# Performance work log

Hardware: AMD Instinct MI355X
Metric: run time of the kernel (lower is better)

The kernel has to match this reference:

```python
import jax, jax.numpy as jnp
import numpy as np

B, T, D, H, O = 256, 256, 256, 1024, 256


def setup_inputs() -> dict:
    key = jax.random.key(0)
    ks = jax.random.split(key, 4)
    x = jax.random.normal(ks[0], (B, T, D), dtype=jnp.float32)
    # Glorot-ish scaling to keep gates/tanh out of saturation
    Wx = jax.random.normal(ks[1], (D + O, 4 * H), dtype=jnp.float32) * 0.05
    Wh = jax.random.normal(ks[2], (H, 4 * H), dtype=jnp.float32) * 0.05
    b = jnp.zeros((4 * H,), dtype=jnp.float32)
    Wd = jax.random.normal(ks[3], (H, O), dtype=jnp.float32) * 0.05
    bd = jnp.zeros((O,), dtype=jnp.float32)
    return {"x": x, "Wx": Wx, "Wh": Wh, "b": b, "Wd": Wd, "bd": bd}


def reference(x, Wx, Wh, b, Wd, bd):
    """Autoregressive LSTM cell unrolled over time with lax.scan.

    Each step: concat(input_t, prev_dense_output) -> LSTMCell (Keras gate
    order i,f,c,o) -> Dense+tanh -> output fed back next step.
    """
    Bz = x.shape[0]
    Hh = Wh.shape[0]
    Oo = Wd.shape[1]
    h0 = jnp.zeros((Bz, Hh), dtype=x.dtype)
    c0 = jnp.zeros((Bz, Hh), dtype=x.dtype)
    y0 = jnp.zeros((Bz, Oo), dtype=x.dtype)  # initial prev_output

    def step(carry, xt):
        h, c, y = carry
        combined = jnp.concatenate([xt, y], axis=-1)  # [B, D+O]
        z = combined @ Wx + h @ Wh + b                # [B, 4H]
        i, f, g, o = jnp.split(z, 4, axis=-1)
        i = jax.nn.sigmoid(i)
        f = jax.nn.sigmoid(f)
        g = jnp.tanh(g)
        o = jax.nn.sigmoid(o)
        c_new = f * c + i * g
        h_new = o * jnp.tanh(c_new)
        y_new = jnp.tanh(h_new @ Wd + bd)             # Dense(tanh)
        return (h_new, c_new, y_new), y_new

    xs = jnp.swapaxes(x, 0, 1)  # [T, B, D]
    _, ys = jax.lax.scan(step, (h0, c0, y0), xs)
    return jnp.swapaxes(ys, 0, 1)  # [B, T, O]
```

## Files before the change

### kernel.cpp

```cpp
#include <hip/hip_runtime.h>


typedef _Float16 f16x8 __attribute__((ext_vector_type(8)));
typedef _Float16 f16x4 __attribute__((ext_vector_type(4)));
typedef float f32x4 __attribute__((ext_vector_type(4)));

#define TSTEPS 256
#define HID 1024
#define OUTD 256
#define KF 1536
#define KA 1280
#define NBLK 256
#define RSLOTS 16
#define SLOTE (256 * KA)

#define RING_OFF   0ull
#define WFULLT_OFF 0ull
#define WDT_OFF    12582912ull
#define XH_OFF     13107200ull
#define FLAGS_OFF  46661632ull
#define WS_NEEDED  46678016ull

#define LDS_SLAB_BYTES 98304
#define LDS_WDT_BYTES  32768
#define LDS_ZBUF_BYTES 16896
#define LDS_TOTAL (LDS_SLAB_BYTES + LDS_WDT_BYTES + LDS_ZBUF_BYTES)

#define AGENT __HIP_MEMORY_SCOPE_AGENT

__device__ __forceinline__ float sigf(float x) {
    return 1.0f / (1.0f + __expf(-x));
}
__device__ __forceinline__ float tanhfast(float x) {
    return 1.0f - 2.0f / (__expf(2.0f * x) + 1.0f);
}

__device__ __forceinline__ void garrive(int* flags, int bid, int ep) {
    __syncthreads();
    if (threadIdx.x == 0)
        __hip_atomic_store(flags + bid * 16, ep, __ATOMIC_RELAXED, AGENT);
}
__device__ __forceinline__ void gwait(int* flags, int ep) {
    if (threadIdx.x < 64) {
        int lane = threadIdx.x;
        for (;;) {
            int a0 = __hip_atomic_load(flags + (lane)       * 16, __ATOMIC_RELAXED, AGENT);
            int a1 = __hip_atomic_load(flags + (lane + 64)  * 16, __ATOMIC_RELAXED, AGENT);
            int a2 = __hip_atomic_load(flags + (lane + 128) * 16, __ATOMIC_RELAXED, AGENT);
            int a3 = __hip_atomic_load(flags + (lane + 192) * 16, __ATOMIC_RELAXED, AGENT);
            int m = min(min(a0, a1), min(a2, a3));
            if (m >= ep) break;
            __builtin_amdgcn_s_sleep(1);
        }
    }
    __syncthreads();
}

__global__ void prep_w(const float* __restrict__ Wx, const float* __restrict__ Wh,
                       const float* __restrict__ Wd,
                       _Float16* __restrict__ WfullT, _Float16* __restrict__ WdT) {
    int bid = blockIdx.x;
    if (bid < 4096) {
        int n = bid;
        for (int k = threadIdx.x; k < KF; k += 256) {
            float v;
            if (k < 256)       v = Wx[(size_t)k * 4096 + n];
            else if (k < 1280) v = Wh[(size_t)(k - 256) * 4096 + n];
            else               v = Wx[(size_t)(k - 1024) * 4096 + n];
            WfullT[(size_t)n * KF + k] = (_Float16)v;
        }
    } else {
        int o = bid - 4096;
        for (int k = threadIdx.x; k < HID; k += 256) {
            WdT[(size_t)o * HID + k] = (_Float16)Wd[(size_t)k * OUTD + o];
        }
    }
}

__global__ void prep_x(const float* __restrict__ x, _Float16* __restrict__ xh, int* flags) {
    size_t i0 = ((size_t)blockIdx.x * 256 + threadIdx.x) * 8;
    float4 a = *(const float4*)(x + i0);
    float4 c = *(const float4*)(x + i0 + 4);
    f16x8 v;
    v[0] = (_Float16)a.x; v[1] = (_Float16)a.y; v[2] = (_Float16)a.z; v[3] = (_Float16)a.w;
    v[4] = (_Float16)c.x; v[5] = (_Float16)c.y; v[6] = (_Float16)c.z; v[7] = (_Float16)c.w;
    *(f16x8*)(xh + i0) = v;
    if (blockIdx.x == 0)
        for (int i = threadIdx.x; i < 4096; i += 256) flags[i] = 0;
}

template<int NS, typename AL>
__device__ __forceinline__ void gemmPart(AL&& aload, const _Float16* slab, int kbB,
                                         int rl, int kg, f32x4 (&acc)[2][2]) {
    constexpr int PFD = (NS < 8) ? NS : 8;
    f16x8 pa[PFD][2];
#pragma unroll
    for (int i = 0; i < PFD; ++i) { pa[i][0] = aload(i, 0); pa[i][1] = aload(i, 1); }
    const int sw = rl & 7;
    const _Float16* bb0 = slab + (size_t)rl * 1536;
    const _Float16* bb1 = slab + (size_t)(16 + rl) * 1536;
#pragma unroll
    for (int kk = 0; kk < NS; ++kk) {
        int kblk = kbB + kk * 4 + kg;
        int idx = (kblk ^ sw) * 8;
        f16x8 b0 = *(const f16x8*)(bb0 + idx);
        f16x8 b1 = *(const f16x8*)(bb1 + idx);
        f16x8 a0 = pa[kk % PFD][0];
        f16x8 a1 = pa[kk % PFD][1];
        if (kk + PFD < NS) {
            pa[kk % PFD][0] = aload(kk + PFD, 0);
            pa[kk % PFD][1] = aload(kk + PFD, 1);
        }
        acc[0][0] = __builtin_amdgcn_mfma_f32_16x16x32_f16(a0, b0, acc[0][0], 0, 0, 0);
        acc[0][1] = __builtin_amdgcn_mfma_f32_16x16x32_f16(a0, b1, acc[0][1], 0, 0, 0);
        acc[1][0] = __builtin_amdgcn_mfma_f32_16x16x32_f16(a1, b0, acc[1][0], 0, 0, 0);
        acc[1][1] = __builtin_amdgcn_mfma_f32_16x16x32_f16(a1, b1, acc[1][1], 0, 0, 0);
    }
}

__global__ __launch_bounds__(256, 1) void lstm_persist(
        const _Float16* __restrict__ WfullT, const _Float16* __restrict__ WdT,
        const _Float16* __restrict__ xh, const float* __restrict__ b,
        const float* __restrict__ bd,
        _Float16* __restrict__ ring,
        int* flags, float* __restrict__ out) {
    extern __shared__ char dynsm[];
    _Float16* slab = (_Float16*)dynsm;
    _Float16* wdt  = (_Float16*)(dynsm + LDS_SLAB_BYTES);
    float* zbuf = (float*)(dynsm + LDS_SLAB_BYTES + LDS_WDT_BYTES);

    const int tid = threadIdx.x, bid = blockIdx.x;
    const int w = tid >> 6, lane = tid & 63;
    const int rl = lane & 15, kg = lane >> 4;

    const int bat0 = (bid >> 7) << 7;
    const int n0 = (bid & 127) << 3;
    const int r0 = (bid >> 4) << 4;
    const int c0 = (bid & 15) << 4;

    for (int i = tid; i < 32 * 192; i += 256) {
        int vcol = i / 192, kblk = i % 192;
        int n = (vcol & 3) * 1024 + n0 + (vcol >> 2);
        f16x8 v = *(const f16x8*)(WfullT + (size_t)n * KF + kblk * 8);
        *(f16x8*)(slab + ((size_t)vcol * 192 + (kblk ^ (vcol & 7))) * 8) = v;
    }
    for (int i = tid; i < 16 * 128; i += 256) {
        int wcol = i >> 7, kb = i & 127;
        f16x8 v = *(const f16x8*)(WdT + (size_t)(c0 + wcol) * HID + kb * 8);
        *(f16x8*)(wdt + ((size_t)wcol * 128 + (kb ^ (wcol & 7))) * 8) = v;
    }
    const int trow = tid >> 1;
    const int ccB = (tid & 1) * 4;
    float bb[4][4];
#pragma unroll
    for (int g = 0; g < 4; ++g)
#pragma unroll
        for (int c2 = 0; c2 < 4; ++c2)
            bb[g][c2] = b[g * 1024 + n0 + ccB + c2];
    const float bdv = bd[c0 + (tid & 15)];
    float creg[4] = {0.f, 0.f, 0.f, 0.f};

    garrive(flags, bid, 1);
    gwait(flags, 1);

    const size_t arow = (size_t)(bat0 + w * 32 + rl);

    for (int t = 0; t < TSTEPS; ++t) {
        if ((t & 7) == 0)
            __builtin_amdgcn_fence(__ATOMIC_ACQUIRE, "agent");

        const _Float16* slotR = ring + (size_t)((t + RSLOTS - 1) & (RSLOTS - 1)) * SLOTE;
        _Float16* slotW = ring + (size_t)(t & (RSLOTS - 1)) * SLOTE;

        f32x4 acc[2][2];
#pragma unroll
        for (int mt = 0; mt < 2; ++mt)
#pragma unroll
            for (int nt = 0; nt < 2; ++nt) {
                acc[mt][nt][0] = 0.f; acc[mt][nt][1] = 0.f;
                acc[mt][nt][2] = 0.f; acc[mt][nt][3] = 0.f;
            }

        {
            const _Float16* xb = xh + arow * 65536 + (size_t)t * 256 + kg * 8;
            auto loadX = [&](int kk, int mt) -> f16x8 {
                return *(const f16x8*)(xb + (size_t)mt * 16 * 65536 + kk * 32);
            };
            gemmPart<8>(loadX, slab, 0, rl, kg, acc);

            if (t > 0) {
                const _Float16* hb = slotR + arow * KA + kg * 8;
                auto loadH = [&](int kk, int mt) -> f16x8 {
                    return *(const f16x8*)(hb + (size_t)mt * 16 * KA + kk * 32);
                };
                gemmPart<32>(loadH, slab, 32, rl, kg, acc);
            }
        }

        gwait(flags, 2 * t + 1);

        if (t > 0) {
            const _Float16* yb = slotR + arow * KA + 1024 + kg * 8;
            auto loadY = [&](int kk, int mt) -> f16x8 {
                return *(const f16x8*)(yb + (size_t)mt * 16 * KA + kk * 32);
            };
            gemmPart<8>(loadY, slab, 160, rl, kg, acc);
        }

#pragma unroll
        for (int mt = 0; mt < 2; ++mt)
#pragma unroll
            for (int nt = 0; nt < 2; ++nt)
#pragma unroll
                for (int r = 0; r < 4; ++r) {
                    int zrow = w * 32 + mt * 16 + kg * 4 + r;
                    zbuf[zrow * 33 + nt * 16 + rl] = acc[mt][nt][r];
                }
        __syncthreads();
        {
            union { f16x4 v; unsigned long long u; } hu;
#pragma unroll
            for (int c2 = 0; c2 < 4; ++c2) {
                int cc = ccB + c2;
                float zi = zbuf[trow * 33 + cc * 4 + 0];
                float zf = zbuf[trow * 33 + cc * 4 + 1];
                float zg = zbuf[trow * 33 + cc * 4 + 2];
                float zo = zbuf[trow * 33 + cc * 4 + 3];
                float iv = sigf(zi + bb[0][c2]);
                float fv = sigf(zf + bb[1][c2]);
                float gv = tanhfast(zg + bb[2][c2]);
                float ov = sigf(zo + bb[3][c2]);
                float cnew = fv * creg[c2] + iv * gv;
                creg[c2] = cnew;
                hu.v[c2] = (_Float16)(ov * tanhfast(cnew));
            }
            __hip_atomic_store(
                (unsigned long long*)(slotW + (size_t)(bat0 + trow) * KA + n0 + ccB),
                hu.u, __ATOMIC_RELAXED, AGENT);
        }

        garrive(flags, bid, 2 * t + 2);
        gwait(flags, 2 * t + 2);

        {
            const _Float16* hp = slotW + (size_t)(r0 + rl) * KA + (w << 8) + kg * 8;
            f16x8 ha[8], wa[8];
#pragma unroll
            for (int it = 0; it < 8; ++it)
                ha[it] = *(const f16x8*)(hp + it * 32);
#pragma unroll
            for (int it = 0; it < 8; ++it) {
                int kb = (w << 5) + it * 4 + kg;
                wa[it] = *(const f16x8*)(wdt + ((size_t)rl * 128 + (kb ^ (rl & 7))) * 8);
            }
            f32x4 accB; accB[0] = 0.f; accB[1] = 0.f; accB[2] = 0.f; accB[3] = 0.f;
#pragma unroll
            for (int it = 0; it < 8; ++it)
                accB = __builtin_amdgcn_mfma_f32_16x16x32_f16(ha[it], wa[it], accB, 0, 0, 0);
            float* red = zbuf;
#pragma unroll
            for (int r = 0; r < 4; ++r)
                red[w * 256 + (kg * 4 + r) * 16 + rl] = accB[r];
            __syncthreads();
            int rr = tid >> 4, cc = tid & 15;
            float s = red[rr * 16 + cc] + red[256 + rr * 16 + cc] +
                      red[512 + rr * 16 + cc] + red[768 + rr * 16 + cc];
            float y = tanhfast(s + bdv);
            __hip_atomic_store(out + (size_t)(r0 + rr) * 65536 + (size_t)t * 256 + (c0 + cc),
                               y, __ATOMIC_RELAXED, AGENT);
            union { _Float16 h; unsigned short u; } cv; cv.h = (_Float16)y;
            unsigned short* ys = (unsigned short*)(zbuf + 1024);
            ys[tid] = cv.u;
            __syncthreads();
            if (tid < 64) {
                unsigned long long yv = *(const unsigned long long*)(ys + tid * 4);
                int row = r0 + (tid >> 2), colb = c0 + (tid & 3) * 4;
                __hip_atomic_store(
                    (unsigned long long*)(slotW + (size_t)row * KA + 1024 + colb),
                    yv, __ATOMIC_RELAXED, AGENT);
            }
        }

        garrive(flags, bid, 2 * t + 3);
    }
}

extern "C" void kernel_launch(void* const* d_in, const int* in_sizes, int n_in,
                              void* d_out, int out_size, void* d_ws, size_t ws_size,
                              hipStream_t stream) {
    const float* x  = (const float*)d_in[0];
    const float* Wx = (const float*)d_in[1];
    const float* Wh = (const float*)d_in[2];
    const float* b  = (const float*)d_in[3];
    const float* Wd = (const float*)d_in[4];
    const float* bd = (const float*)d_in[5];
    float* out = (float*)d_out;
    char* ws = (char*)d_ws;
    if (ws_size < WS_NEEDED) return;

    _Float16* WfullT = (_Float16*)(ws + WFULLT_OFF);
    _Float16* WdT    = (_Float16*)(ws + WDT_OFF);
    _Float16* xh     = (_Float16*)(ws + XH_OFF);
    _Float16* ring   = (_Float16*)(ws + RING_OFF);
    int*      flags  = (int*)(ws + FLAGS_OFF);

    static int lds_set = 0;
    if (!lds_set) {
        hipFuncSetAttribute((const void*)lstm_persist,
                            hipFuncAttributeMaxDynamicSharedMemorySize, LDS_TOTAL);
        lds_set = 1;
    }

    prep_w<<<4352, 256, 0, stream>>>(Wx, Wh, Wd, WfullT, WdT);
    prep_x<<<8192, 256, 0, stream>>>(x, xh, flags);
    lstm_persist<<<NBLK, 256, LDS_TOTAL, stream>>>(WfullT, WdT, xh, b, bd, ring, flags, out);
}
```

Measured before the change: 4.832 ms.

## Restructure LSTM step schedule with split h/y flags and half-grid barriers

Reorders each timestep so the dense output phase runs right after h is published. The next step's h-GEMM then overlaps with the y exchange. Separate flag arrays for h and y are used, and each block waits only on the 128 blocks of its batch half instead of all 256. Flags are packed densely instead of padded per cache line, with longer sleep intervals in the polling loops. The aim is to cut global barrier latency per step, at the risk of flag-line contention from the dense packing and coarser wake-up from the longer sleep.

Result: faster. 4.259 ms (-11.9%).

```diff
diff --git a/kernel.cpp b/kernel.cpp
--- a/kernel.cpp
+++ b/kernel.cpp
@@ -19,7 +19,7 @@
 #define WDT_OFF    12582912ull
 #define XH_OFF     13107200ull
 #define FLAGS_OFF  46661632ull
-#define WS_NEEDED  46678016ull
+#define WS_NEEDED  46663680ull
 
 #define LDS_SLAB_BYTES 98304
 #define LDS_WDT_BYTES  32768
@@ -38,19 +38,30 @@
 __device__ __forceinline__ void garrive(int* flags, int bid, int ep) {
     __syncthreads();
     if (threadIdx.x == 0)
-        __hip_atomic_store(flags + bid * 16, ep, __ATOMIC_RELAXED, AGENT);
-}
-__device__ __forceinline__ void gwait(int* flags, int ep) {
+        __hip_atomic_store(flags + bid, ep, __ATOMIC_RELAXED, AGENT);
+}
+__device__ __forceinline__ void gwait(int* flags, int gbase, int ep) {
     if (threadIdx.x < 64) {
         int lane = threadIdx.x;
         for (;;) {
-            int a0 = __hip_atomic_load(flags + (lane)       * 16, __ATOMIC_RELAXED, AGENT);
-            int a1 = __hip_atomic_load(flags + (lane + 64)  * 16, __ATOMIC_RELAXED, AGENT);
-            int a2 = __hip_atomic_load(flags + (lane + 128) * 16, __ATOMIC_RELAXED, AGENT);
-            int a3 = __hip_atomic_load(flags + (lane + 192) * 16, __ATOMIC_RELAXED, AGENT);
-            int m = min(min(a0, a1), min(a2, a3));
-            if (m >= ep) break;
-            __builtin_amdgcn_s_sleep(1);
+            int a0 = __hip_atomic_load(flags + gbase + lane,      __ATOMIC_RELAXED, AGENT);
+            int a1 = __hip_atomic_load(flags + gbase + 64 + lane, __ATOMIC_RELAXED, AGENT);
+            if (min(a0, a1) >= ep) break;
+            __builtin_amdgcn_s_sleep(8);
+        }
+    }
+    __syncthreads();
+}
+__device__ __forceinline__ void gwait256(int* flags, int ep) {
+    if (threadIdx.x < 64) {
+        int lane = threadIdx.x;
+        for (;;) {
+            int a0 = __hip_atomic_load(flags + lane,       __ATOMIC_RELAXED, AGENT);
+            int a1 = __hip_atomic_load(flags + lane + 64,  __ATOMIC_RELAXED, AGENT);
+            int a2 = __hip_atomic_load(flags + lane + 128, __ATOMIC_RELAXED, AGENT);
+            int a3 = __hip_atomic_load(flags + lane + 192, __ATOMIC_RELAXED, AGENT);
+            if (min(min(a0, a1), min(a2, a3)) >= ep) break;
+            __builtin_amdgcn_s_sleep(8);
         }
     }
     __syncthreads();
@@ -85,8 +96,10 @@
     v[0] = (_Float16)a.x; v[1] = (_Float16)a.y; v[2] = (_Float16)a.z; v[3] = (_Float16)a.w;
     v[4] = (_Float16)c.x; v[5] = (_Float16)c.y; v[6] = (_Float16)c.z; v[7] = (_Float16)c.w;
     *(f16x8*)(xh + i0) = v;
-    if (blockIdx.x == 0)
-        for (int i = threadIdx.x; i < 4096; i += 256) flags[i] = 0;
+    if (blockIdx.x == 0) {
+        flags[threadIdx.x] = 0;
+        flags[256 + threadIdx.x] = 0;
+    }
 }
 
 template<int NS, typename AL>
@@ -137,6 +150,10 @@
     const int n0 = (bid & 127) << 3;
     const int r0 = (bid >> 4) << 4;
     const int c0 = (bid & 15) << 4;
+    const int gbase = bid & 128;
+
+    int* hflags = flags;
+    int* yflags = flags + 256;
 
     for (int i = tid; i < 32 * 192; i += 256) {
         int vcol = i / 192, kblk = i % 192;
@@ -160,19 +177,105 @@
     const float bdv = bd[c0 + (tid & 15)];
     float creg[4] = {0.f, 0.f, 0.f, 0.f};
 
-    garrive(flags, bid, 1);
-    gwait(flags, 1);
-
     const size_t arow = (size_t)(bat0 + w * 32 + rl);
+
+    auto epilogue = [&](f32x4 (&A)[2][2], _Float16* slotW) {
+#pragma unroll
+        for (int mt = 0; mt < 2; ++mt)
+#pragma unroll
+            for (int nt = 0; nt < 2; ++nt)
+#pragma unroll
+                for (int r = 0; r < 4; ++r) {
+                    int zrow = w * 32 + mt * 16 + kg * 4 + r;
+                    zbuf[zrow * 33 + nt * 16 + rl] = A[mt][nt][r];
+                }
+        __syncthreads();
+        union { f16x4 v; unsigned long long u; } hu;
+#pragma unroll
+        for (int c2 = 0; c2 < 4; ++c2) {
+            int cc = ccB + c2;
+            float zi = zbuf[trow * 33 + cc * 4 + 0];
+            float zf = zbuf[trow * 33 + cc * 4 + 1];
+            float zg = zbuf[trow * 33 + cc * 4 + 2];
+            float zo = zbuf[trow * 33 + cc * 4 + 3];
+            float iv = sigf(zi + bb[0][c2]);
+            float fv = sigf(zf + bb[1][c2]);
+            float gv = tanhfast(zg + bb[2][c2]);
+            float ov = sigf(zo + bb[3][c2]);
+            float cnew = fv * creg[c2] + iv * gv;
+            creg[c2] = cnew;
+            hu.v[c2] = (_Float16)(ov * tanhfast(cnew));
+        }
+        __hip_atomic_store(
+            (unsigned long long*)(slotW + (size_t)(bat0 + trow) * KA + n0 + ccB),
+            hu.u, __ATOMIC_RELAXED, AGENT);
+    };
+
+    auto phaseB = [&](int t, _Float16* slotT) {
+        const _Float16* hp = slotT + (size_t)(r0 + rl) * KA + (w << 8) + kg * 8;
+        f16x8 ha[8], wa[8];
+#pragma unroll
+        for (int it = 0; it < 8; ++it)
+            ha[it] = *(const f16x8*)(hp + it * 32);
+#pragma unroll
+        for (int it = 0; it < 8; ++it) {
+            int kb = (w << 5) + it * 4 + kg;
+            wa[it] = *(const f16x8*)(wdt + ((size_t)rl * 128 + (kb ^ (rl & 7))) * 8);
+        }
+        f32x4 accB; accB[0] = 0.f; accB[1] = 0.f; accB[2] = 0.f; accB[3] = 0.f;
+#pragma unroll
+        for (int it = 0; it < 8; ++it)
+            accB = __builtin_amdgcn_mfma_f32_16x16x32_f16(ha[it], wa[it], accB, 0, 0, 0);
+        float* red = zbuf;
+#pragma unroll
+        for (int r = 0; r < 4; ++r)
+            red[w * 256 + (kg * 4 + r) * 16 + rl] = accB[r];
+        __syncthreads();
+        int rr = tid >> 4, cc = tid & 15;
+        float s = red[rr * 16 + cc] + red[256 + rr * 16 + cc] +
+                  red[512 + rr * 16 + cc] + red[768 + rr * 16 + cc];
+        float y = tanhfast(s + bdv);
+        out[(size_t)(r0 + rr) * 65536 + (size_t)t * 256 + (c0 + cc)] = y;
+        union { _Float16 h; unsigned short u; } cv; cv.h = (_Float16)y;
+        unsigned short* ys = (unsigned short*)(zbuf + 1024);
+        ys[tid] = cv.u;
+        __syncthreads();
+        if (tid < 64) {
+            unsigned long long yv = *(const unsigned long long*)(ys + tid * 4);
+            int row = r0 + (tid >> 2), colb = c0 + (tid & 3) * 4;
+            __hip_atomic_store(
+                (unsigned long long*)(slotT + (size_t)row * KA + 1024 + colb),
+                yv, __ATOMIC_RELAXED, AGENT);
+        }
+    };
+
+    garrive(hflags, bid, 1);
+    gwait256(hflags, 1);
+
+    f32x4 acc[2][2];
+#pragma unroll
+    for (int mt = 0; mt < 2; ++mt)
+#pragma unroll
+        for (int nt = 0; nt < 2; ++nt) {
+            acc[mt][nt][0] = 0.f; acc[mt][nt][1] = 0.f;
+            acc[mt][nt][2] = 0.f; acc[mt][nt][3] = 0.f;
+        }
+    {
+        const _Float16* xb = xh + arow * 65536 + kg * 8;
+        auto loadX = [&](int kk, int mt) -> f16x8 {
+            return *(const f16x8*)(xb + (size_t)mt * 16 * 65536 + kk * 32);
+        };
+        gemmPart<8>(loadX, slab, 0, rl, kg, acc);
+    }
+    epilogue(acc, ring);
+    garrive(hflags, bid, 2);
 
     for (int t = 0; t < TSTEPS; ++t) {
         if ((t & 7) == 0)
             __builtin_amdgcn_fence(__ATOMIC_ACQUIRE, "agent");
 
-        const _Float16* slotR = ring + (size_t)((t + RSLOTS - 1) & (RSLOTS - 1)) * SLOTE;
-        _Float16* slotW = ring + (size_t)(t & (RSLOTS - 1)) * SLOTE;
-
-        f32x4 acc[2][2];
+        _Float16* slotT = ring + (size_t)(t & (RSLOTS - 1)) * SLOTE;
+
 #pragma unroll
         for (int mt = 0; mt < 2; ++mt)
 #pragma unroll
@@ -181,107 +284,41 @@
                 acc[mt][nt][2] = 0.f; acc[mt][nt][3] = 0.f;
             }
 
-        {
-            const _Float16* xb = xh + arow * 65536 + (size_t)t * 256 + kg * 8;
+        if (t < TSTEPS - 1) {
+            const _Float16* xb = xh + arow * 65536 + (size_t)(t + 1) * 256 + kg * 8;
             auto loadX = [&](int kk, int mt) -> f16x8 {
                 return *(const f16x8*)(xb + (size_t)mt * 16 * 65536 + kk * 32);
             };
             gemmPart<8>(loadX, slab, 0, rl, kg, acc);
-
-            if (t > 0) {
-                const _Float16* hb = slotR + arow * KA + kg * 8;
+        }
+
+        gwait(hflags, gbase, t + 2);
+        phaseB(t, slotT);
+
+        if (t < TSTEPS - 1) {
+            garrive(yflags, bid, t + 1);
+
+            {
+                const _Float16* hb = slotT + arow * KA + kg * 8;
                 auto loadH = [&](int kk, int mt) -> f16x8 {
                     return *(const f16x8*)(hb + (size_t)mt * 16 * KA + kk * 32);
                 };
                 gemmPart<32>(loadH, slab, 32, rl, kg, acc);
             }
-        }
-
-        gwait(flags, 2 * t + 1);
-
-        if (t > 0) {
-            const _Float16* yb = slotR + arow * KA + 1024 + kg * 8;
-            auto loadY = [&](int kk, int mt) -> f16x8 {
-                return *(const f16x8*)(yb + (size_t)mt * 16 * KA + kk * 32);
-            };
-            gemmPart<8>(loadY, slab, 160, rl, kg, acc);
-        }
-
-#pragma unroll
-        for (int mt = 0; mt < 2; ++mt)
-#pragma unroll
-            for (int nt = 0; nt < 2; ++nt)
-#pragma unroll
-                for (int r = 0; r < 4; ++r) {
-                    int zrow = w * 32 + mt * 16 + kg * 4 + r;
-                    zbuf[zrow * 33 + nt * 16 + rl] = acc[mt][nt][r];
-                }
-        __syncthreads();
-        {
-            union { f16x4 v; unsigned long long u; } hu;
-#pragma unroll
-            for (int c2 = 0; c2 < 4; ++c2) {
-                int cc = ccB + c2;
-                float zi = zbuf[trow * 33 + cc * 4 + 0];
-                float zf = zbuf[trow * 33 + cc * 4 + 1];
-                float zg = zbuf[trow * 33 + cc * 4 + 2];
-                float zo = zbuf[trow * 33 + cc * 4 + 3];
-                float iv = sigf(zi + bb[0][c2]);
-                float fv = sigf(zf + bb[1][c2]);
-                float gv = tanhfast(zg + bb[2][c2]);
-                float ov = sigf(zo + bb[3][c2]);
-                float cnew = fv * creg[c2] + iv * gv;
-                creg[c2] = cnew;
-                hu.v[c2] = (_Float16)(ov * tanhfast(cnew));
+
+            gwait(yflags, gbase, t + 1);
+
+            {
+                const _Float16* yb = slotT + arow * KA + 1024 + kg * 8;
+                auto loadY = [&](int kk, int mt) -> f16x8 {
+                    return *(const f16x8*)(yb + (size_t)mt * 16 * KA + kk * 32);
+                };
+                gemmPart<8>(loadY, slab, 160, rl, kg, acc);
             }
-            __hip_atomic_store(
-                (unsigned long long*)(slotW + (size_t)(bat0 + trow) * KA + n0 + ccB),
-                hu.u, __ATOMIC_RELAXED, AGENT);
-        }
-
-        garrive(flags, bid, 2 * t + 2);
-        gwait(flags, 2 * t + 2);
-
-        {
-            const _Float16* hp = slotW + (size_t)(r0 + rl) * KA + (w << 8) + kg * 8;
-            f16x8 ha[8], wa[8];
-#pragma unroll
-            for (int it = 0; it < 8; ++it)
-                ha[it] = *(const f16x8*)(hp + it * 32);
-#pragma unroll
-            for (int it = 0; it < 8; ++it) {
-                int kb = (w << 5) + it * 4 + kg;
-                wa[it] = *(const f16x8*)(wdt + ((size_t)rl * 128 + (kb ^ (rl & 7))) * 8);
-            }
-            f32x4 accB; accB[0] = 0.f; accB[1] = 0.f; accB[2] = 0.f; accB[3] = 0.f;
-#pragma unroll
-            for (int it = 0; it < 8; ++it)
-                accB = __builtin_amdgcn_mfma_f32_16x16x32_f16(ha[it], wa[it], accB, 0, 0, 0);
-            float* red = zbuf;
-#pragma unroll
-            for (int r = 0; r < 4; ++r)
-                red[w * 256 + (kg * 4 + r) * 16 + rl] = accB[r];
-            __syncthreads();
-            int rr = tid >> 4, cc = tid & 15;
-            float s = red[rr * 16 + cc] + red[256 + rr * 16 + cc] +
-                      red[512 + rr * 16 + cc] + red[768 + rr * 16 + cc];
-            float y = tanhfast(s + bdv);
-            __hip_atomic_store(out + (size_t)(r0 + rr) * 65536 + (size_t)t * 256 + (c0 + cc),
-                               y, __ATOMIC_RELAXED, AGENT);
-            union { _Float16 h; unsigned short u; } cv; cv.h = (_Float16)y;
-            unsigned short* ys = (unsigned short*)(zbuf + 1024);
-            ys[tid] = cv.u;
-            __syncthreads();
-            if (tid < 64) {
-                unsigned long long yv = *(const unsigned long long*)(ys + tid * 4);
-                int row = r0 + (tid >> 2), colb = c0 + (tid & 3) * 4;
-                __hip_atomic_store(
-                    (unsigned long long*)(slotW + (size_t)row * KA + 1024 + colb),
-                    yv, __ATOMIC_RELAXED, AGENT);
-            }
-        }
-
-        garrive(flags, bid, 2 * t + 3);
+
+            epilogue(acc, ring + (size_t)((t + 1) & (RSLOTS - 1)) * SLOTE);
+            garrive(hflags, bid, t + 3);
+        }
     }
 }
 
```
